# Optimization experiments

Hardware: AMD Instinct MI355X
Metric: run time of the kernel (lower is better)

The kernel has to match this reference:

```python
import jax, jax.numpy as jnp
import numpy as np

EMBED_DIM = 1024
NUM_MEMORY_SLOTS = 256
B, Q = 8, 4096


def setup_inputs() -> dict:
    key = jax.random.key(0)
    ks = jax.random.split(key, 6)
    s = 1.0 / np.sqrt(EMBED_DIM)
    return {
        "x": jax.random.normal(ks[0], (B, Q, EMBED_DIM), dtype=jnp.float32),
        "memory_bank": jax.random.normal(ks[1], (NUM_MEMORY_SLOTS, EMBED_DIM), dtype=jnp.float32),
        "Wq": jax.random.uniform(ks[2], (EMBED_DIM, EMBED_DIM), jnp.float32, -s, s),
        "bq": jax.random.uniform(ks[3], (EMBED_DIM,), jnp.float32, -s, s),
        "Wo": jax.random.uniform(ks[4], (EMBED_DIM, EMBED_DIM), jnp.float32, -s, s),
        "bo": jax.random.uniform(ks[5], (EMBED_DIM,), jnp.float32, -s, s),
    }


def reference(x, memory_bank, Wq, bq, Wo, bo):
    # query projection: [B,Q,E]
    queries = jnp.einsum('bqe,fe->bqf', x, Wq) + bq
    # attention over fixed memory bank: scores [B,Q,M]
    scores = jnp.einsum('bqe,me->bqm', queries, memory_bank)
    weights = jax.nn.softmax(scores, axis=-1)
    attended = jnp.einsum('bqm,me->bqe', weights, memory_bank)
    # output projection + residual
    return jnp.einsum('bqe,fe->bqf', attended, Wo) + bo + x
```

## Files before the change

### kernel.cpp

```cpp
#include <hip/hip_runtime.h>
#include <hip/hip_bf16.h>
#include <stdint.h>

#define TOK 32768
#define EMB 1024
#define MSL 256

typedef __attribute__((ext_vector_type(8))) short short8;
typedef __attribute__((ext_vector_type(4))) float f32x4;

#define SBAR() asm volatile("s_waitcnt lgkmcnt(0)\n\ts_barrier" ::: "memory")

__device__ __forceinline__ ushort f2bf(float f) {
    union { float f; uint32_t u; } c; c.f = f;
    uint32_t u = c.u;
    return (ushort)((u + 0x7fffu + ((u >> 16) & 1u)) >> 16);
}

__device__ __forceinline__ void split2(float f, ushort& h, ushort& l) {
    union { float f; uint32_t u; } c; c.f = f;
    h = (ushort)(c.u >> 16);
    union { uint32_t u; float f; } hv; hv.u = c.u & 0xffff0000u;
    union { float f; uint32_t u; } lc; lc.f = f - hv.f;
    l = (ushort)(lc.u >> 16);
}

__device__ __forceinline__ void async_copy16(const void* gsrc, void* ldst) {
    __builtin_amdgcn_global_load_lds(
        (const __attribute__((address_space(1))) uint32_t*)gsrc,
        (__attribute__((address_space(3))) uint32_t*)ldst,
        16, 0, 0);
}


__global__ __launch_bounds__(256) void pre_small(
    const float* __restrict__ Wq, ushort* __restrict__ wqth, ushort* __restrict__ wqtl,
    const float* __restrict__ mb, ushort* __restrict__ mbh, ushort* __restrict__ mbl,
    const float* __restrict__ bq, float* __restrict__ cvec)
{
    __shared__ float ld[64 * 65];
    const int b = blockIdx.x;
    const int t = threadIdx.x;
    if (b < 256) {
        const int eBase = (b & 15) * 64;
        const int fBase = (b >> 4) * 64;
        #pragma unroll
        for (int r = 0; r < 16; ++r) {
            int row = r * 4 + (t >> 6);
            int col = t & 63;
            ld[row * 65 + col] = Wq[(size_t)(fBase + row) * EMB + eBase + col];
        }
        __syncthreads();
        #pragma unroll
        for (int r = 0; r < 16; ++r) {
            int row = r * 4 + (t >> 6);
            int col = t & 63;
            float v = ld[col * 65 + row];
            ushort h, l; split2(v, h, l);
            size_t o = (size_t)(eBase + row) * EMB + fBase + col;
            wqth[o] = h; wqtl[o] = l;
        }
    } else if (b < 512) {
        int i = (b - 256) * 256 + t;
        float4 v = ((const float4*)mb)[i];
        ushort4 h4, l4;
        split2(v.x, h4.x, l4.x); split2(v.y, h4.y, l4.y);
        split2(v.z, h4.z, l4.z); split2(v.w, h4.w, l4.w);
        ((ushort4*)mbh)[i] = h4;
        ((ushort4*)mbl)[i] = l4;
    } else {
        int m = (b - 512) * 4 + (t >> 6);
        int lane = t & 63;
        const float4* mrow = (const float4*)(mb + (size_t)m * EMB);
        const float4* brow = (const float4*)bq;
        float s = 0.f;
        #pragma unroll
        for (int k = 0; k < 4; ++k) {
            float4 a = mrow[lane + k * 64];
            float4 bb = brow[lane + k * 64];
            s += a.x * bb.x + a.y * bb.y + a.z * bb.z + a.w * bb.w;
        }
        #pragma unroll
        for (int off = 32; off; off >>= 1) s += __shfl_xor(s, off, 64);
        if (lane == 0) cvec[m] = s;
    }
}

template<int MODE>
__device__ __forceinline__ void gemm_body(
    ushort* smem, const float* __restrict__ A,
    const ushort* __restrict__ Bh, const ushort* __restrict__ Bl,
    ushort* __restrict__ O1, ushort* __restrict__ O2,
    int K, int bx, int by)
{
    ushort* sAh = smem;
    ushort* sAl = smem + 8192;
    ushort* sBh = smem + 16384;
    ushort* sBl = smem + 24576;

    const int t = threadIdx.x;
    const int lane = t & 63;
    const int wave = t >> 6;
    const int wr = wave >> 1;
    const int wc = wave & 1;
    const int rowBase = by * 128;
    const int colBase = bx * 128;

    const float*  Ab  = A  + (size_t)rowBase * K;
    const ushort* Bhb = Bh + (size_t)colBase * K;
    const ushort* Blb = Bl + (size_t)colBase * K;

    const int cg = ((t & 7) ^ ((t >> 3) & 7)) << 3;

    f32x4 acc[4][4] = {};

    const int kIters = K >> 6;
    for (int kt = 0; kt < kIters; ++kt) {
        const int k0 = kt << 6;
        __syncthreads();
        #pragma unroll
        for (int r = 0; r < 4; ++r) {
            int row = r * 32 + (t >> 3);
            async_copy16(Bhb + (size_t)row * K + k0 + cg, &sBh[(size_t)(r * 256 + wave * 64) * 8]);
            async_copy16(Blb + (size_t)row * K + k0 + cg, &sBl[(size_t)(r * 256 + wave * 64) * 8]);
        }
        #pragma unroll
        for (int r = 0; r < 4; ++r) {
            int i = r * 256 + t;
            int row = r * 32 + (t >> 3);
            const float* src = Ab + (size_t)row * K + k0 + cg;
            float4 f0 = *(const float4*)src;
            float4 f1 = *(const float4*)(src + 4);
            short8 hv, lv; ushort h, l;
            split2(f0.x, h, l); hv[0] = (short)h; lv[0] = (short)l;
            split2(f0.y, h, l); hv[1] = (short)h; lv[1] = (short)l;
            split2(f0.z, h, l); hv[2] = (short)h; lv[2] = (short)l;
            split2(f0.w, h, l); hv[3] = (short)h; lv[3] = (short)l;
            split2(f1.x, h, l); hv[4] = (short)h; lv[4] = (short)l;
            split2(f1.y, h, l); hv[5] = (short)h; lv[5] = (short)l;
            split2(f1.z, h, l); hv[6] = (short)h; lv[6] = (short)l;
            split2(f1.w, h, l); hv[7] = (short)h; lv[7] = (short)l;
            *(short8*)&sAh[(size_t)i * 8] = hv;
            *(short8*)&sAl[(size_t)i * 8] = lv;
        }
        __syncthreads();

        #pragma unroll
        for (int ks = 0; ks < 2; ++ks) {
            const int kc = ks * 4 + (lane >> 4);
            short8 ah[4], al[4], bh[4], bl[4];
            #pragma unroll
            for (int i2 = 0; i2 < 4; ++i2) {
                int row = wr * 64 + i2 * 16 + (lane & 15);
                int off = row * 64 + ((kc ^ (row & 7)) << 3);
                ah[i2] = *(const short8*)&sAh[off];
                al[i2] = *(const short8*)&sAl[off];
            }
            #pragma unroll
            for (int j = 0; j < 4; ++j) {
                int row = wc * 64 + j * 16 + (lane & 15);
                int off = row * 64 + ((kc ^ (row & 7)) << 3);
                bh[j] = *(const short8*)&sBh[off];
                bl[j] = *(const short8*)&sBl[off];
            }
            #pragma unroll
            for (int i2 = 0; i2 < 4; ++i2)
                #pragma unroll
                for (int j = 0; j < 4; ++j) {
                    acc[i2][j] = __builtin_amdgcn_mfma_f32_16x16x32_bf16(ah[i2], bh[j], acc[i2][j], 0, 0, 0);
                    acc[i2][j] = __builtin_amdgcn_mfma_f32_16x16x32_bf16(ah[i2], bl[j], acc[i2][j], 0, 0, 0);
                    acc[i2][j] = __builtin_amdgcn_mfma_f32_16x16x32_bf16(al[i2], bh[j], acc[i2][j], 0, 0, 0);
                }
        }
    }

    #pragma unroll
    for (int i2 = 0; i2 < 4; ++i2) {
        #pragma unroll
        for (int j = 0; j < 4; ++j) {
            const int col = colBase + wc * 64 + j * 16 + (lane & 15);
            #pragma unroll
            for (int r = 0; r < 4; ++r) {
                const int row = rowBase + wr * 64 + i2 * 16 + ((lane >> 4) << 2) + r;
                float v = acc[i2][j][r];
                if (MODE == 0) {
                    int ktx = col >> 6, kcc = (col >> 3) & 7;
                    int ksx = kcc >> 2, lh = kcc & 3, e = col & 7;
                    int wcj = row >> 4, ll = row & 15;
                    size_t idx = (((size_t)(ktx * 2 + ksx) * 16 + wcj) * 64 + lh * 16 + ll) * 8 + e;
                    ushort h, l; split2(v, h, l);
                    O1[idx] = h;
                    O2[idx] = l;
                } else {
                    int fc = row >> 6, jj = (row & 63) >> 4, lanelo = row & 15;
                    int cc = col >> 3, ksx = cc >> 2, lanehi = cc & 3, e = col & 7;
                    size_t idx = ((((size_t)fc * 8 + ksx) * 4 + jj) * 64 + lanehi * 16 + lanelo) * 8 + e;
                    O1[idx] = f2bf(v);
                }
            }
        }
    }
}

__global__ __launch_bounds__(256) void pre_gemms(
    const float* __restrict__ mb, const ushort* __restrict__ wqth, const ushort* __restrict__ wqtl,
    const float* __restrict__ Wo, const ushort* __restrict__ mbh, const ushort* __restrict__ mbl,
    ushort* __restrict__ Pfh, ushort* __restrict__ Pfl, ushort* __restrict__ RTfrag)
{
    __shared__ ushort smem[32768];
    const int b = blockIdx.x;
    if (b < 16) {
        gemm_body<0>(smem, mb, wqth, wqtl, Pfh, Pfl, EMB, b & 7, b >> 3);
    } else {
        const int id = b - 16;
        gemm_body<1>(smem, Wo, mbh, mbl, RTfrag, nullptr, EMB, id & 1, id >> 1);
    }
}

__global__ __launch_bounds__(256, 3) void fused_attn(
    const float* __restrict__ x, const ushort* __restrict__ Pfh,
    const ushort* __restrict__ Pfl, const float* __restrict__ cvec,
    const ushort* __restrict__ RTfrag, const float* __restrict__ bo,
    float* __restrict__ out)
{
    __shared__ ushort smem[17408];
    ushort* sW  = smem;
    float*  redM = (float*)&smem[16384];
    float*  redS = (float*)&smem[16896];

    const int t = threadIdx.x;
    const int lane = t & 63;
    const int wave = t >> 6;
    const int wc = wave;
    const int rowBase = blockIdx.x * 64;

    const float* Ab = x + (size_t)rowBase * EMB;
    const int cg = ((t & 7) ^ ((t >> 3) & 7)) << 3;

    f32x4 acc[4][4] = {};
    float4 xr[2][2];

    auto loadX = [&](int kt) {
        const int k0 = kt << 6;
        #pragma unroll
        for (int r = 0; r < 2; ++r) {
            const float* src = Ab + (size_t)(r * 32 + (t >> 3)) * EMB + k0 + cg;
            xr[r][0] = *(const float4*)src;
            xr[r][1] = *(const float4*)(src + 4);
        }
    };

    loadX(0);

    for (int kt = 0; kt < 16; ++kt) {
        ushort* bufAh = smem + (kt & 1) * 8192;
        ushort* bufAl = bufAh + 4096;
        #pragma unroll
        for (int r = 0; r < 2; ++r) {
            int i = r * 256 + t;
            short8 hv, lv; ushort h, l;
            split2(xr[r][0].x, h, l); hv[0] = (short)h; lv[0] = (short)l;
            split2(xr[r][0].y, h, l); hv[1] = (short)h; lv[1] = (short)l;
            split2(xr[r][0].z, h, l); hv[2] = (short)h; lv[2] = (short)l;
            split2(xr[r][0].w, h, l); hv[3] = (short)h; lv[3] = (short)l;
            split2(xr[r][1].x, h, l); hv[4] = (short)h; lv[4] = (short)l;
            split2(xr[r][1].y, h, l); hv[5] = (short)h; lv[5] = (short)l;
            split2(xr[r][1].z, h, l); hv[6] = (short)h; lv[6] = (short)l;
            split2(xr[r][1].w, h, l); hv[7] = (short)h; lv[7] = (short)l;
            *(short8*)&bufAh[(size_t)i * 8] = hv;
            *(short8*)&bufAl[(size_t)i * 8] = lv;
        }
        if (kt < 15) loadX(kt + 1);
        SBAR();

        #pragma unroll
        for (int ks = 0; ks < 2; ++ks) {
            const int kc = ks * 4 + (lane >> 4);
            short8 ah[4], al[4], bh[4], bl[4];
            #pragma unroll
            for (int i2 = 0; i2 < 4; ++i2) {
                int row = i2 * 16 + (lane & 15);
                int off = row * 64 + ((kc ^ (row & 7)) << 3);
                ah[i2] = *(const short8*)&bufAh[off];
                al[i2] = *(const short8*)&bufAl[off];
            }
            #pragma unroll
            for (int j = 0; j < 4; ++j) {
                size_t boff = ((size_t)((kt * 2 + ks) * 16 + wc * 4 + j) * 64 + lane) * 8;
                bh[j] = *(const short8*)&Pfh[boff];
                bl[j] = *(const short8*)&Pfl[boff];
            }
            #pragma unroll
            for (int i2 = 0; i2 < 4; ++i2)
                #pragma unroll
                for (int j = 0; j < 4; ++j) {
                    acc[i2][j] = __builtin_amdgcn_mfma_f32_16x16x32_bf16(ah[i2], bh[j], acc[i2][j], 0, 0, 0);
                    acc[i2][j] = __builtin_amdgcn_mfma_f32_16x16x32_bf16(ah[i2], bl[j], acc[i2][j], 0, 0, 0);
                    acc[i2][j] = __builtin_amdgcn_mfma_f32_16x16x32_bf16(al[i2], bh[j], acc[i2][j], 0, 0, 0);
                }
        }
    }

    {
        float cj[4];
        #pragma unroll
        for (int j = 0; j < 4; ++j) cj[j] = cvec[wc * 64 + j * 16 + (lane & 15)];
        #pragma unroll
        for (int i2 = 0; i2 < 4; ++i2)
            #pragma unroll
            for (int j = 0; j < 4; ++j)
                #pragma unroll
                for (int r = 0; r < 4; ++r) acc[i2][j][r] += cj[j];
    }
    float pmax[4][4];
    #pragma unroll
    for (int i2 = 0; i2 < 4; ++i2)
        #pragma unroll
        for (int r = 0; r < 4; ++r) {
            float m0 = fmaxf(fmaxf(acc[i2][0][r], acc[i2][1][r]),
                             fmaxf(acc[i2][2][r], acc[i2][3][r]));
            #pragma unroll
            for (int off = 8; off; off >>= 1) m0 = fmaxf(m0, __shfl_xor(m0, off, 64));
            pmax[i2][r] = m0;
        }
    __syncthreads();
    if ((lane & 15) == 0) {
        #pragma unroll
        for (int i2 = 0; i2 < 4; ++i2)
            #pragma unroll
            for (int r = 0; r < 4; ++r)
                redM[wc * 64 + i2 * 16 + ((lane >> 4) << 2) + r] = pmax[i2][r];
    }
    __syncthreads();
    {
        float psum[4][4];
        #pragma unroll
        for (int i2 = 0; i2 < 4; ++i2)
            #pragma unroll
            for (int r = 0; r < 4; ++r) {
                int R = i2 * 16 + ((lane >> 4) << 2) + r;
                float mx = fmaxf(fmaxf(redM[R], redM[64 + R]),
                                 fmaxf(redM[128 + R], redM[192 + R]));
                float s = 0.f;
                #pragma unroll
                for (int j = 0; j < 4; ++j) {
                    float e = __expf(acc[i2][j][r] - mx);
                    acc[i2][j][r] = e;
                    s += e;
                }
                #pragma unroll
                for (int off = 8; off; off >>= 1) s += __shfl_xor(s, off, 64);
                psum[i2][r] = s;
            }
        if ((lane & 15) == 0) {
            #pragma unroll
            for (int i2 = 0; i2 < 4; ++i2)
                #pragma unroll
                for (int r = 0; r < 4; ++r)
                    redS[wc * 64 + i2 * 16 + ((lane >> 4) << 2) + r] = psum[i2][r];
        }
    }
    __syncthreads();
    #pragma unroll
    for (int i2 = 0; i2 < 4; ++i2)
        #pragma unroll
        for (int r = 0; r < 4; ++r) {
            int R = i2 * 16 + ((lane >> 4) << 2) + r;
            float tot = redS[R] + redS[64 + R] + redS[128 + R] + redS[192 + R];
            float inv = 1.0f / tot;
            #pragma unroll
            for (int j = 0; j < 4; ++j) {
                int col = wc * 64 + j * 16 + (lane & 15);
                int cc = col >> 3;
                int slot = (cc & 24) | ((cc & 7) ^ (R & 7));
                sW[R * 256 + slot * 8 + (lane & 7)] = f2bf(acc[i2][j][r] * inv);
            }
        }
    __syncthreads();

    const int wr2 = wave >> 1;
    const int wc2 = wave & 1;

    short8 af[2][8];
    #pragma unroll
    for (int i2 = 0; i2 < 2; ++i2) {
        int R = wr2 * 32 + i2 * 16 + (lane & 15);
        #pragma unroll
        for (int ks = 0; ks < 8; ++ks) {
            int cc = ks * 4 + (lane >> 4);
            int slot = (cc & 24) | ((cc & 7) ^ (R & 7));
            af[i2][ks] = *(const short8*)&sW[R * 256 + slot * 8];
        }
    }

    for (int fc = 0; fc < 16; ++fc) {
        f32x4 acc2[2][2] = {};
        #pragma unroll
        for (int ks = 0; ks < 8; ++ks) {
            short8 b[2];
            #pragma unroll
            for (int j = 0; j < 2; ++j) {
                int jj = wc2 * 2 + j;
                b[j] = *(const short8*)&RTfrag[((((size_t)fc * 8 + ks) * 4 + jj) * 64 + lane) * 8];
            }
            #pragma unroll
            for (int i2 = 0; i2 < 2; ++i2)
                #pragma unroll
                for (int j = 0; j < 2; ++j)
                    acc2[i2][j] = __builtin_amdgcn_mfma_f32_16x16x32_bf16(
                        af[i2][ks], b[j], acc2[i2][j], 0, 0, 0);
        }
        #pragma unroll
        for (int i2 = 0; i2 < 2; ++i2)
            #pragma unroll
            for (int j = 0; j < 2; ++j) {
                int col = fc * 64 + wc2 * 32 + j * 16 + (lane & 15);
                float bcol = bo[col];
                #pragma unroll
                for (int r = 0; r < 4; ++r) {
                    int row = rowBase + wr2 * 32 + i2 * 16 + ((lane >> 4) << 2) + r;
                    out[(size_t)row * EMB + col] =
                        acc2[i2][j][r] + bcol + x[(size_t)row * EMB + col];
                }
            }
    }
}

extern "C" void kernel_launch(void* const* d_in, const int* in_sizes, int n_in,
                              void* d_out, int out_size, void* d_ws, size_t ws_size,
                              hipStream_t stream) {
    const float* x  = (const float*)d_in[0];
    const float* mb = (const float*)d_in[1];
    const float* Wq = (const float*)d_in[2];
    const float* bq = (const float*)d_in[3];
    const float* Wo = (const float*)d_in[4];
    const float* bo = (const float*)d_in[5];
    float* out = (float*)d_out;

    char* ws = (char*)d_ws;
    size_t o = 0;
    ushort* mbh    = (ushort*)(ws + o); o += (size_t)MSL * EMB * 2;
    ushort* mbl    = (ushort*)(ws + o); o += (size_t)MSL * EMB * 2;
    ushort* wqth   = (ushort*)(ws + o); o += (size_t)EMB * EMB * 2;
    ushort* wqtl   = (ushort*)(ws + o); o += (size_t)EMB * EMB * 2;
    ushort* Pfh    = (ushort*)(ws + o); o += (size_t)MSL * EMB * 2;
    ushort* Pfl    = (ushort*)(ws + o); o += (size_t)MSL * EMB * 2;
    ushort* RTfrag = (ushort*)(ws + o); o += (size_t)EMB * MSL * 2;
    float*  cvec   = (float*)(ws + o);  o += (size_t)MSL * 4;

    pre_small<<<576, 256, 0, stream>>>(Wq, wqth, wqtl, mb, mbh, mbl, bq, cvec);

    pre_gemms<<<32, 256, 0, stream>>>(mb, wqth, wqtl, Wo, mbh, mbl, Pfh, Pfl, RTfrag);

    fused_attn<<<TOK / 64, 256, 0, stream>>>(x, Pfh, Pfl, cvec, RTfrag, bo, out);
}
```

Baseline: 368.5 us.

## Split fused attention block across eight waves instead of four

The fused attention kernel now runs 512 threads per block, eight waves, on the same 64-row tile. Each wave covers half as many score columns in the first GEMM and half as many output rows in the second, and the softmax reductions combine eight partial results instead of four. The aim is to cut per-wave register use and serial MFMA chains and raise the number of waves resident per CU. The cost is that each wave reloads the shared A fragments from LDS with less reuse per load, and cross-wave reduction and barrier traffic increases.

```diff
diff --git a/kernel.cpp b/kernel.cpp
--- a/kernel.cpp
+++ b/kernel.cpp
@@ -217,16 +217,16 @@
     }
 }
 
-__global__ __launch_bounds__(256, 3) void fused_attn(
+__global__ __launch_bounds__(512, 4) void fused_attn(
     const float* __restrict__ x, const ushort* __restrict__ Pfh,
     const ushort* __restrict__ Pfl, const float* __restrict__ cvec,
     const ushort* __restrict__ RTfrag, const float* __restrict__ bo,
     float* __restrict__ out)
 {
-    __shared__ ushort smem[17408];
+    __shared__ ushort smem[18432];
     ushort* sW  = smem;
     float*  redM = (float*)&smem[16384];
-    float*  redS = (float*)&smem[16896];
+    float*  redS = (float*)&smem[17408];
 
     const int t = threadIdx.x;
     const int lane = t & 63;
@@ -237,17 +237,14 @@
     const float* Ab = x + (size_t)rowBase * EMB;
     const int cg = ((t & 7) ^ ((t >> 3) & 7)) << 3;
 
-    f32x4 acc[4][4] = {};
-    float4 xr[2][2];
+    f32x4 acc[4][2] = {};
+    float4 xr[2];
 
     auto loadX = [&](int kt) {
         const int k0 = kt << 6;
-        #pragma unroll
-        for (int r = 0; r < 2; ++r) {
-            const float* src = Ab + (size_t)(r * 32 + (t >> 3)) * EMB + k0 + cg;
-            xr[r][0] = *(const float4*)src;
-            xr[r][1] = *(const float4*)(src + 4);
-        }
+        const float* src = Ab + (size_t)(t >> 3) * EMB + k0 + cg;
+        xr[0] = *(const float4*)src;
+        xr[1] = *(const float4*)(src + 4);
     };
 
     loadX(0);
@@ -255,20 +252,18 @@
     for (int kt = 0; kt < 16; ++kt) {
         ushort* bufAh = smem + (kt & 1) * 8192;
         ushort* bufAl = bufAh + 4096;
-        #pragma unroll
-        for (int r = 0; r < 2; ++r) {
-            int i = r * 256 + t;
+        {
             short8 hv, lv; ushort h, l;
-            split2(xr[r][0].x, h, l); hv[0] = (short)h; lv[0] = (short)l;
-            split2(xr[r][0].y, h, l); hv[1] = (short)h; lv[1] = (short)l;
-            split2(xr[r][0].z, h, l); hv[2] = (short)h; lv[2] = (short)l;
-            split2(xr[r][0].w, h, l); hv[3] = (short)h; lv[3] = (short)l;
-            split2(xr[r][1].x, h, l); hv[4] = (short)h; lv[4] = (short)l;
-            split2(xr[r][1].y, h, l); hv[5] = (short)h; lv[5] = (short)l;
-            split2(xr[r][1].z, h, l); hv[6] = (short)h; lv[6] = (short)l;
-            split2(xr[r][1].w, h, l); hv[7] = (short)h; lv[7] = (short)l;
-            *(short8*)&bufAh[(size_t)i * 8] = hv;
-            *(short8*)&bufAl[(size_t)i * 8] = lv;
+            split2(xr[0].x, h, l); hv[0] = (short)h; lv[0] = (short)l;
+            split2(xr[0].y, h, l); hv[1] = (short)h; lv[1] = (short)l;
+            split2(xr[0].z, h, l); hv[2] = (short)h; lv[2] = (short)l;
+            split2(xr[0].w, h, l); hv[3] = (short)h; lv[3] = (short)l;
+            split2(xr[1].x, h, l); hv[4] = (short)h; lv[4] = (short)l;
+            split2(xr[1].y, h, l); hv[5] = (short)h; lv[5] = (short)l;
+            split2(xr[1].z, h, l); hv[6] = (short)h; lv[6] = (short)l;
+            split2(xr[1].w, h, l); hv[7] = (short)h; lv[7] = (short)l;
+            *(short8*)&bufAh[(size_t)t * 8] = hv;
+            *(short8*)&bufAl[(size_t)t * 8] = lv;
         }
         if (kt < 15) loadX(kt + 1);
         SBAR();
@@ -276,39 +271,37 @@
         #pragma unroll
         for (int ks = 0; ks < 2; ++ks) {
             const int kc = ks * 4 + (lane >> 4);
-            short8 ah[4], al[4], bh[4], bl[4];
+            short8 bh[2], bl[2];
+            #pragma unroll
+            for (int j = 0; j < 2; ++j) {
+                size_t boff = ((size_t)((kt * 2 + ks) * 16 + wc * 2 + j) * 64 + lane) * 8;
+                bh[j] = *(const short8*)&Pfh[boff];
+                bl[j] = *(const short8*)&Pfl[boff];
+            }
             #pragma unroll
             for (int i2 = 0; i2 < 4; ++i2) {
                 int row = i2 * 16 + (lane & 15);
                 int off = row * 64 + ((kc ^ (row & 7)) << 3);
-                ah[i2] = *(const short8*)&bufAh[off];
-                al[i2] = *(const short8*)&bufAl[off];
-            }
-            #pragma unroll
-            for (int j = 0; j < 4; ++j) {
-                size_t boff = ((size_t)((kt * 2 + ks) * 16 + wc * 4 + j) * 64 + lane) * 8;
-                bh[j] = *(const short8*)&Pfh[boff];
-                bl[j] = *(const short8*)&Pfl[boff];
-            }
-            #pragma unroll
-            for (int i2 = 0; i2 < 4; ++i2)
-                #pragma unroll
-                for (int j = 0; j < 4; ++j) {
-                    acc[i2][j] = __builtin_amdgcn_mfma_f32_16x16x32_bf16(ah[i2], bh[j], acc[i2][j], 0, 0, 0);
-                    acc[i2][j] = __builtin_amdgcn_mfma_f32_16x16x32_bf16(ah[i2], bl[j], acc[i2][j], 0, 0, 0);
-                    acc[i2][j] = __builtin_amdgcn_mfma_f32_16x16x32_bf16(al[i2], bh[j], acc[i2][j], 0, 0, 0);
+                short8 ah = *(const short8*)&bufAh[off];
+                short8 al = *(const short8*)&bufAl[off];
+                #pragma unroll
+                for (int j = 0; j < 2; ++j) {
+                    acc[i2][j] = __builtin_amdgcn_mfma_f32_16x16x32_bf16(ah, bh[j], acc[i2][j], 0, 0, 0);
+                    acc[i2][j] = __builtin_amdgcn_mfma_f32_16x16x32_bf16(ah, bl[j], acc[i2][j], 0, 0, 0);
+                    acc[i2][j] = __builtin_amdgcn_mfma_f32_16x16x32_bf16(al, bh[j], acc[i2][j], 0, 0, 0);
                 }
+            }
         }
     }
 
     {
-        float cj[4];
-        #pragma unroll
-        for (int j = 0; j < 4; ++j) cj[j] = cvec[wc * 64 + j * 16 + (lane & 15)];
+        float cj[2];
+        #pragma unroll
+        for (int j = 0; j < 2; ++j) cj[j] = cvec[wc * 32 + j * 16 + (lane & 15)];
         #pragma unroll
         for (int i2 = 0; i2 < 4; ++i2)
             #pragma unroll
-            for (int j = 0; j < 4; ++j)
+            for (int j = 0; j < 2; ++j)
                 #pragma unroll
                 for (int r = 0; r < 4; ++r) acc[i2][j][r] += cj[j];
     }
@@ -317,8 +310,7 @@
     for (int i2 = 0; i2 < 4; ++i2)
         #pragma unroll
         for (int r = 0; r < 4; ++r) {
-            float m0 = fmaxf(fmaxf(acc[i2][0][r], acc[i2][1][r]),
-                             fmaxf(acc[i2][2][r], acc[i2][3][r]));
+            float m0 = fmaxf(acc[i2][0][r], acc[i2][1][r]);
             #pragma unroll
             for (int off = 8; off; off >>= 1) m0 = fmaxf(m0, __shfl_xor(m0, off, 64));
             pmax[i2][r] = m0;
@@ -339,11 +331,12 @@
             #pragma unroll
             for (int r = 0; r < 4; ++r) {
                 int R = i2 * 16 + ((lane >> 4) << 2) + r;
-                float mx = fmaxf(fmaxf(redM[R], redM[64 + R]),
-                                 fmaxf(redM[128 + R], redM[192 + R]));
+                float mx = redM[R];
+                #pragma unroll
+                for (int w2 = 1; w2 < 8; ++w2) mx = fmaxf(mx, redM[w2 * 64 + R]);
                 float s = 0.f;
                 #pragma unroll
-                for (int j = 0; j < 4; ++j) {
+                for (int j = 0; j < 2; ++j) {
                     float e = __expf(acc[i2][j][r] - mx);
                     acc[i2][j][r] = e;
                     s += e;
@@ -366,11 +359,13 @@
         #pragma unroll
         for (int r = 0; r < 4; ++r) {
             int R = i2 * 16 + ((lane >> 4) << 2) + r;
-            float tot = redS[R] + redS[64 + R] + redS[128 + R] + redS[192 + R];
+            float tot = redS[R];
+            #pragma unroll
+            for (int w2 = 1; w2 < 8; ++w2) tot += redS[w2 * 64 + R];
             float inv = 1.0f / tot;
             #pragma unroll
-            for (int j = 0; j < 4; ++j) {
-                int col = wc * 64 + j * 16 + (lane & 15);
+            for (int j = 0; j < 2; ++j) {
+                int col = wc * 32 + j * 16 + (lane & 15);
                 int cc = col >> 3;
                 int slot = (cc & 24) | ((cc & 7) ^ (R & 7));
                 sW[R * 256 + slot * 8 + (lane & 7)] = f2bf(acc[i2][j][r] * inv);
@@ -381,20 +376,19 @@
     const int wr2 = wave >> 1;
     const int wc2 = wave & 1;
 
-    short8 af[2][8];
-    #pragma unroll
-    for (int i2 = 0; i2 < 2; ++i2) {
-        int R = wr2 * 32 + i2 * 16 + (lane & 15);
+    short8 af[8];
+    {
+        int R = wr2 * 16 + (lane & 15);
         #pragma unroll
         for (int ks = 0; ks < 8; ++ks) {
             int cc = ks * 4 + (lane >> 4);
             int slot = (cc & 24) | ((cc & 7) ^ (R & 7));
-            af[i2][ks] = *(const short8*)&sW[R * 256 + slot * 8];
+            af[ks] = *(const short8*)&sW[R * 256 + slot * 8];
         }
     }
 
     for (int fc = 0; fc < 16; ++fc) {
-        f32x4 acc2[2][2] = {};
+        f32x4 acc2[2] = {};
         #pragma unroll
         for (int ks = 0; ks < 8; ++ks) {
             short8 b[2];
@@ -404,25 +398,20 @@
                 b[j] = *(const short8*)&RTfrag[((((size_t)fc * 8 + ks) * 4 + jj) * 64 + lane) * 8];
             }
             #pragma unroll
-            for (int i2 = 0; i2 < 2; ++i2)
-                #pragma unroll
-                for (int j = 0; j < 2; ++j)
-                    acc2[i2][j] = __builtin_amdgcn_mfma_f32_16x16x32_bf16(
-                        af[i2][ks], b[j], acc2[i2][j], 0, 0, 0);
-        }
-        #pragma unroll
-        for (int i2 = 0; i2 < 2; ++i2)
-            #pragma unroll
-            for (int j = 0; j < 2; ++j) {
-                int col = fc * 64 + wc2 * 32 + j * 16 + (lane & 15);
-                float bcol = bo[col];
-                #pragma unroll
-                for (int r = 0; r < 4; ++r) {
-                    int row = rowBase + wr2 * 32 + i2 * 16 + ((lane >> 4) << 2) + r;
-                    out[(size_t)row * EMB + col] =
-                        acc2[i2][j][r] + bcol + x[(size_t)row * EMB + col];
-                }
-            }
+            for (int j = 0; j < 2; ++j)
+                acc2[j] = __builtin_amdgcn_mfma_f32_16x16x32_bf16(af[ks], b[j], acc2[j], 0, 0, 0);
+        }
+        #pragma unroll
+        for (int j = 0; j < 2; ++j) {
+            int col = fc * 64 + wc2 * 32 + j * 16 + (lane & 15);
+            float bcol = bo[col];
+            #pragma unroll
+            for (int r = 0; r < 4; ++r) {
+                int row = rowBase + wr2 * 16 + ((lane >> 4) << 2) + r;
+                out[(size_t)row * EMB + col] =
+                    acc2[j][r] + bcol + x[(size_t)row * EMB + col];
+            }
+        }
     }
 }
 
@@ -452,5 +441,5 @@
 
     pre_gemms<<<32, 256, 0, stream>>>(mb, wqth, wqtl, Wo, mbh, mbl, Pfh, Pfl, RTfrag);
 
-    fused_attn<<<TOK / 64, 256, 0, stream>>>(x, Pfh, Pfl, cvec, RTfrag, bo, out);
-}
+    fused_attn<<<TOK / 64, 512, 0, stream>>>(x, Pfh, Pfl, cvec, RTfrag, bo, out);
+}
```

Measured after the change: 355.5 us. 1.04x faster.
